# Kernel optimization log

Hardware: AMD Instinct MI355X
Metric: run time of the kernel (lower is better)

## Reference

```python
import jax, jax.numpy as jnp
import numpy as np

B = 8
A = 180      # num_angles
D = 512      # det_count
IMG = 512    # img_size


def _forward(x):
    # --- Ram-Lak filter in frequency domain ---
    freq = jnp.abs(jnp.fft.rfftfreq(D)).astype(jnp.float32)            # [D//2+1]
    filtered = jnp.fft.irfft(jnp.fft.rfft(x, axis=-1) * freq, n=D, axis=-1)  # [B,A,D]

    # --- precompute per-angle detector coordinates for every pixel ---
    lin = jnp.linspace(-1.0, 1.0, IMG, dtype=jnp.float32)
    yy, xx = jnp.meshgrid(lin, lin, indexing='ij')
    xxf = xx.reshape(-1)                                               # [HW]
    yyf = yy.reshape(-1)
    angles = jnp.linspace(0.0, np.pi - np.pi / A, A, dtype=jnp.float32)
    t = (xxf[None, :] * jnp.cos(angles)[:, None]
         + yyf[None, :] * jnp.sin(angles)[:, None]) / np.sqrt(2.0)     # [A,HW]
    u = jnp.clip((t + 1.0) * 0.5 * (D - 1.0), 0.0, D - 1.0)
    idx0 = jnp.floor(u).astype(jnp.int32)
    idx1 = jnp.minimum(idx0 + 1, D - 1)
    w = u - idx0.astype(jnp.float32)

    # --- backprojection sweep: scan over angles, accumulate in-register ---
    proj = jnp.transpose(filtered, (1, 0, 2))                          # [A,B,D]

    def step(acc, inputs):
        p, i0, i1, wa = inputs                                         # p:[B,D], i*/wa:[HW]
        s = jnp.take(p, i0, axis=1) * (1.0 - wa) + jnp.take(p, i1, axis=1) * wa
        return acc + s, None

    bn = x.shape[0]
    acc0 = jnp.zeros((bn, IMG * IMG), dtype=jnp.float32)
    acc, _ = jax.lax.scan(step, acc0, (proj, idx0, idx1, w))

    det_pixel_size = 2.0 / float(D)
    fbp = acc.reshape(bn, 1, IMG, IMG) * (det_pixel_size * np.pi / float(A))

    # --- 3x3 gaussian blur (sigma=0.5), depthwise on single channel ---
    coords = jnp.arange(-1, 2, dtype=jnp.float32)
    k1 = jnp.exp(-0.5 * (coords / 0.5) ** 2)
    k1 = k1 / k1.sum()
    k2 = jnp.outer(k1, k1)[None, None]                                 # [1,1,3,3] OIHW
    fbp = jax.lax.conv_general_dilated(fbp, k2, (1, 1), 'SAME')
    return jnp.clip(fbp, -1.0, 1.0)


def setup_inputs() -> dict:
    key = jax.random.key(0)
    x = jax.random.normal(key, (B, A, D), dtype=jnp.float32)
    return {"x": x, "input_is_sinogram": 1}


def reference(x, input_is_sinogram):
    # input_is_sinogram is a constant flag (True path): x is the sinogram [B,A,D].
    return _forward(x)
```

## Files before the change

### kernel.cpp

```cpp
#include <hip/hip_runtime.h>
#include <hip/hip_fp16.h>
#include <math.h>

#define NDET 512
#define NANG 180
#define NB   8
#define NIMG 512

#define WS_CASA 0
#define WS_CBT  360
#define WS_FGH  46464
#define WS_BP   (46464 + 368640)

typedef _Float16 h2_t __attribute__((ext_vector_type(2)));

__device__ __forceinline__ void gld_lds16(const void* g, void* l) {
    __builtin_amdgcn_global_load_lds((__attribute__((address_space(1))) void*)g,
                                     (__attribute__((address_space(3))) void*)l,
                                     16, 0, 0);
}

__device__ __forceinline__ int hswz(int s) {
    return (s & 0x78) | ((s ^ (s >> 3)) & 7);
}

__global__ __launch_bounds__(256) void k_filter(const float* __restrict__ x, float* ws) {
    __shared__ float xs[8 * 516];
    __shared__ float hrs[512];
    const int a     = blockIdx.x >> 1;
    const int half_ = blockIdx.x & 1;
    const int tid   = threadIdx.x;
    const int lane  = tid & 63;
    const int wv    = tid >> 6;

    #pragma unroll
    for (int p = 0; p < 2; ++p) {
        int n = tid + 256 * p;
        float h;
        if (n == 0) h = 0.25f;
        else if ((n & 1) == 0) h = 0.0f;
        else {
            double th = (double)n * (M_PI / 256.0);
            double s2 = sin(0.5 * th);
            double S  = (254.0 - 256.0 * cos(th)) / (4.0 * s2 * s2);
            h = (float)((2.0 * S - 256.0) / 262144.0);
        }
        hrs[hswz(n >> 2) * 4 + (n & 3)] = h;
    }
    {
        int b  = wv * 2 + (lane >> 5);
        int l5 = lane & 31;
        const float* xr = x + (b * NANG + a) * NDET;
        float* xd = xs + b * 516;
        #pragma unroll
        for (int p = 0; p < 4; ++p) {
            int idx = l5 * 4 + p * 128;
            *(float4*)(xd + idx) = *(const float4*)(xr + idx);
        }
    }
    if (half_ == 0) {
        double th = (double)a * (M_PI / 180.0);
        double sc = 255.5 / sqrt(2.0);
        const float ca = (float)(cos(th) * sc), sa = (float)(sin(th) * sc);
        if (tid == 0) {
            ws[WS_CASA + 2 * a]     = ca;
            ws[WS_CASA + 2 * a + 1] = sa;
        }
        const int bx = tid & 15, by = tid >> 4;
        const float x0 = -1.f + (float)(bx * 32)      * (2.f / 511.f);
        const float x1 = -1.f + (float)(bx * 32 + 31) * (2.f / 511.f);
        const float y0 = -1.f + (float)(by * 32)      * (2.f / 511.f);
        const float y1 = -1.f + (float)(by * 32 + 31) * (2.f / 511.f);
        float u00 = fmaf(x0, ca, fmaf(y0, sa, 255.5f));
        float u01 = fmaf(x1, ca, fmaf(y0, sa, 255.5f));
        float u10 = fmaf(x0, ca, fmaf(y1, sa, 255.5f));
        float u11 = fmaf(x1, ca, fmaf(y1, sa, 255.5f));
        float umin = fminf(fminf(u00, u01), fminf(u10, u11));
        int d0 = (int)floorf(umin) - 1;
        d0 = max(0, min(476, d0));
        ws[WS_CBT + tid * 180 + a] = 255.5f - (float)d0;
    }
    __syncthreads();

    const int b  = lane & 7;
    const int t  = lane >> 3;
    const int n0 = half_ * 256 + wv * 64 + t * 8;
    const int q  = n0 >> 2;
    const float* xrow = xs + b * 516;

    float acc[8] = {0, 0, 0, 0, 0, 0, 0, 0};
    float win[12];
    {
        int s2 = (-q - 2) & 127;
        int s1 = (-q - 1) & 127;
        float4 h2 = *(const float4*)(hrs + hswz(s2) * 4);
        float4 h1 = *(const float4*)(hrs + hswz(s1) * 4);
        win[0] = h2.x; win[1] = h2.y; win[2]  = h2.z; win[3]  = h2.w;
        win[4] = h1.x; win[5] = h1.y; win[6]  = h1.z; win[7]  = h1.w;
    }
    #pragma unroll 2
    for (int c = 0; c < 128; ++c) {
        int s = (c - q) & 127;
        float4 hc = *(const float4*)(hrs + hswz(s) * 4);
        win[8] = hc.x; win[9] = hc.y; win[10] = hc.z; win[11] = hc.w;
        float4 xv = *(const float4*)(xrow + c * 4);
        float xa[4] = {xv.x, xv.y, xv.z, xv.w};
        #pragma unroll
        for (int k = 0; k < 8; ++k)
            #pragma unroll
            for (int j = 0; j < 4; ++j)
                acc[k] = fmaf(xa[j], win[8 + j - k], acc[k]);
        #pragma unroll
        for (int i2 = 0; i2 < 8; ++i2) win[i2] = win[i2 + 4];
    }
    __half* fgh = (__half*)(ws + WS_FGH);
    #pragma unroll
    for (int k = 0; k < 8; ++k)
        fgh[(a * NDET + n0 + k) * NB + b] = __float2half(acc[k]);
}

#define WWIN 36
#define NCHK (NANG * WWIN)

__global__ __launch_bounds__(1024) void k_bp(float* ws) {
    __shared__ uint4 win4[NCHK];
    const int tid  = threadIdx.x;
    const int wv   = tid >> 6, lane = tid & 63;
    const int bid  = blockIdx.x;
    const int bx   = bid & 15, by = bid >> 4;
    const int iy   = by * 32 + (wv >> 2) * 8 + (lane >> 3);
    const int ix   = bx * 32 + (wv & 3) * 8 + (lane & 7);
    const float xf = -1.0f + (float)ix * (2.0f / 511.0f);
    const float yf = -1.0f + (float)iy * (2.0f / 511.0f);

    const __half* __restrict__ fgh  = (const __half*)(ws + WS_FGH);
    const float*  __restrict__ cbt  = ws + WS_CBT + bid * 180;
    const float*  __restrict__ casa = ws + WS_CASA;

    #pragma unroll
    for (int r = 0; r < 7; ++r) {
        int c = r * 1024 + tid;
        if (c < NCHK) {
            unsigned a = (unsigned)c / 36u;
            int o  = c - (int)a * 36;
            float cb = cbt[a];
            int d0 = (int)(255.5f - cb);
            gld_lds16(fgh + ((int)a * NDET + d0 + o) * NB, win4 + c);
        }
    }
    __syncthreads();

    float acc[8] = {0, 0, 0, 0, 0, 0, 0, 0};
    #pragma unroll 4
    for (int al = 0; al < NANG; ++al) {
        const float2 cs = *(const float2*)(casa + 2 * al);
        const float  cb = cbt[al];
        float v = fmaf(xf, cs.x, fmaf(yf, cs.y, cb));
        v = __builtin_amdgcn_fmed3f(v, 0.0f, 34.99996948f);
        float fj = floorf(v);
        float w  = v - fj;
        int  j0  = (int)fj;
        const char* pc = (const char*)win4 + al * (WWIN * 16) + (j0 << 4);
        uint4 da = *(const uint4*)pc;
        uint4 db = *(const uint4*)(pc + 16);
#if __has_builtin(__builtin_amdgcn_fdot2) && __has_builtin(__builtin_amdgcn_perm) && __has_builtin(__builtin_amdgcn_cvt_pkrtz)
        h2_t wp = __builtin_bit_cast(h2_t, __builtin_amdgcn_cvt_pkrtz(1.0f - w, w));
        unsigned pl0 = __builtin_amdgcn_perm(db.x, da.x, 0x05040100u);
        unsigned ph0 = __builtin_amdgcn_perm(db.x, da.x, 0x07060302u);
        unsigned pl1 = __builtin_amdgcn_perm(db.y, da.y, 0x05040100u);
        unsigned ph1 = __builtin_amdgcn_perm(db.y, da.y, 0x07060302u);
        unsigned pl2 = __builtin_amdgcn_perm(db.z, da.z, 0x05040100u);
        unsigned ph2 = __builtin_amdgcn_perm(db.z, da.z, 0x07060302u);
        unsigned pl3 = __builtin_amdgcn_perm(db.w, da.w, 0x05040100u);
        unsigned ph3 = __builtin_amdgcn_perm(db.w, da.w, 0x07060302u);
        acc[0] = __builtin_amdgcn_fdot2(__builtin_bit_cast(h2_t, pl0), wp, acc[0], false);
        acc[1] = __builtin_amdgcn_fdot2(__builtin_bit_cast(h2_t, ph0), wp, acc[1], false);
        acc[2] = __builtin_amdgcn_fdot2(__builtin_bit_cast(h2_t, pl1), wp, acc[2], false);
        acc[3] = __builtin_amdgcn_fdot2(__builtin_bit_cast(h2_t, ph1), wp, acc[3], false);
        acc[4] = __builtin_amdgcn_fdot2(__builtin_bit_cast(h2_t, pl2), wp, acc[4], false);
        acc[5] = __builtin_amdgcn_fdot2(__builtin_bit_cast(h2_t, ph2), wp, acc[5], false);
        acc[6] = __builtin_amdgcn_fdot2(__builtin_bit_cast(h2_t, pl3), wp, acc[6], false);
        acc[7] = __builtin_amdgcn_fdot2(__builtin_bit_cast(h2_t, ph3), wp, acc[7], false);
#else
        __half2 w2 = __float2half2_rn(w);
        __half2 a0 = __builtin_bit_cast(__half2, da.x), b0 = __builtin_bit_cast(__half2, db.x);
        __half2 a1 = __builtin_bit_cast(__half2, da.y), b1 = __builtin_bit_cast(__half2, db.y);
        __half2 a2 = __builtin_bit_cast(__half2, da.z), b2 = __builtin_bit_cast(__half2, db.z);
        __half2 a3 = __builtin_bit_cast(__half2, da.w), b3 = __builtin_bit_cast(__half2, db.w);
        float2 f0 = __half22float2(__hfma2(w2, __hsub2(b0, a0), a0));
        float2 f1 = __half22float2(__hfma2(w2, __hsub2(b1, a1), a1));
        float2 f2 = __half22float2(__hfma2(w2, __hsub2(b2, a2), a2));
        float2 f3 = __half22float2(__hfma2(w2, __hsub2(b3, a3), a3));
        acc[0] += f0.x; acc[1] += f0.y;
        acc[2] += f1.x; acc[3] += f1.y;
        acc[4] += f2.x; acc[5] += f2.y;
        acc[6] += f3.x; acc[7] += f3.y;
#endif
    }

    const float scale = (float)((2.0 / 512.0) * M_PI / 180.0);
    float* bp = ws + WS_BP;
    #pragma unroll
    for (int b = 0; b < 8; ++b)
        bp[b * (NIMG * NIMG) + iy * NIMG + ix] = acc[b] * scale;
}

__global__ __launch_bounds__(256) void k_blur(const float* __restrict__ ws, float* __restrict__ out) {
    const int gid = blockIdx.x * 256 + threadIdx.x;
    const int b  = gid >> 18;
    const int r  = (gid >> 9) & 511;
    const int cx = gid & 511;
    const float KA = 0.10650697891920077f;
    const float KB = 0.78698604216159850f;
    const float* img = ws + WS_BP + b * (NIMG * NIMG);
    const float* rp = img + r * 512 + cx;

    float rowm = 0.0f, row0, rowp = 0.0f;
    {
        float l  = (cx > 0)   ? rp[-1] : 0.0f;
        float rr = (cx < 511) ? rp[1]  : 0.0f;
        row0 = KA * (l + rr) + KB * rp[0];
    }
    if (r > 0) {
        const float* q = rp - 512;
        float l  = (cx > 0)   ? q[-1] : 0.0f;
        float rr = (cx < 511) ? q[1]  : 0.0f;
        rowm = KA * (l + rr) + KB * q[0];
    }
    if (r < 511) {
        const float* q = rp + 512;
        float l  = (cx > 0)   ? q[-1] : 0.0f;
        float rr = (cx < 511) ? q[1]  : 0.0f;
        rowp = KA * (l + rr) + KB * q[0];
    }
    float v = KA * (rowm + rowp) + KB * row0;
    v = fminf(fmaxf(v, -1.0f), 1.0f);
    out[gid] = v;
}

extern "C" void kernel_launch(void* const* d_in, const int* in_sizes, int n_in,
                              void* d_out, int out_size, void* d_ws, size_t ws_size,
                              hipStream_t stream) {
    const float* x = (const float*)d_in[0];
    float* out = (float*)d_out;
    float* ws  = (float*)d_ws;

    k_filter<<<NANG * 2, 256, 0, stream>>>(x, ws);
    k_bp<<<256, 1024, 0, stream>>>(ws);
    k_blur<<<(NB * NIMG * NIMG) / 256, 256, 0, stream>>>(ws, out);
}
```

Baseline: 77.90 us.

## Split backprojection angles across two blocks per tile with atomic accumulation

Each 32x32 pixel tile's angle loop is now split into two halves of 90 angles, which doubles the grid to 512 blocks. Each block stages half as much LDS window data, and its partial sums go into a zero-initialised buffer through atomicAdd. The detector window is also tightened from 36 to 34 entries by removing the -1 margin. The intent is better CU occupancy and smaller LDS footprint, at the cost of an extra memset, atomic traffic, and a tighter window that could clip edge samples.

```diff
diff --git a/kernel.cpp b/kernel.cpp
--- a/kernel.cpp
+++ b/kernel.cpp
@@ -76,8 +76,8 @@
         float u10 = fmaf(x0, ca, fmaf(y1, sa, 255.5f));
         float u11 = fmaf(x1, ca, fmaf(y1, sa, 255.5f));
         float umin = fminf(fminf(u00, u01), fminf(u10, u11));
-        int d0 = (int)floorf(umin) - 1;
-        d0 = max(0, min(476, d0));
+        int d0 = (int)floorf(umin);
+        d0 = max(0, min(NDET - 34, d0));
         ws[WS_CBT + tid * 180 + a] = 255.5f - (float)d0;
     }
     __syncthreads();
@@ -119,51 +119,54 @@
         fgh[(a * NDET + n0 + k) * NB + b] = __float2half(acc[k]);
 }
 
-#define WWIN 36
-#define NCHK (NANG * WWIN)
-
-__global__ __launch_bounds__(1024) void k_bp(float* ws) {
+#define WWIN 34
+#define CHANG 90
+#define NCHK (CHANG * WWIN)
+
+__global__ __launch_bounds__(1024, 8) void k_bp(float* ws) {
     __shared__ uint4 win4[NCHK];
     const int tid  = threadIdx.x;
     const int wv   = tid >> 6, lane = tid & 63;
-    const int bid  = blockIdx.x;
-    const int bx   = bid & 15, by = bid >> 4;
+    const int tile = blockIdx.x & 255;
+    const int ah   = (blockIdx.x >> 8) * CHANG;
+    const int bx   = tile & 15, by = tile >> 4;
     const int iy   = by * 32 + (wv >> 2) * 8 + (lane >> 3);
     const int ix   = bx * 32 + (wv & 3) * 8 + (lane & 7);
     const float xf = -1.0f + (float)ix * (2.0f / 511.0f);
     const float yf = -1.0f + (float)iy * (2.0f / 511.0f);
 
     const __half* __restrict__ fgh  = (const __half*)(ws + WS_FGH);
-    const float*  __restrict__ cbt  = ws + WS_CBT + bid * 180;
+    const float*  __restrict__ cbt  = ws + WS_CBT + tile * 180;
     const float*  __restrict__ casa = ws + WS_CASA;
 
     #pragma unroll
-    for (int r = 0; r < 7; ++r) {
+    for (int r = 0; r < 3; ++r) {
         int c = r * 1024 + tid;
         if (c < NCHK) {
-            unsigned a = (unsigned)c / 36u;
-            int o  = c - (int)a * 36;
-            float cb = cbt[a];
+            unsigned a = (unsigned)c / 34u;
+            int o  = c - (int)a * 34;
+            int ag = ah + (int)a;
+            float cb = cbt[ag];
             int d0 = (int)(255.5f - cb);
-            gld_lds16(fgh + ((int)a * NDET + d0 + o) * NB, win4 + c);
+            gld_lds16(fgh + (ag * NDET + d0 + o) * NB, win4 + c);
         }
     }
     __syncthreads();
 
     float acc[8] = {0, 0, 0, 0, 0, 0, 0, 0};
     #pragma unroll 4
-    for (int al = 0; al < NANG; ++al) {
-        const float2 cs = *(const float2*)(casa + 2 * al);
-        const float  cb = cbt[al];
+    for (int al = 0; al < CHANG; ++al) {
+        const int ag = ah + al;
+        const float2 cs = *(const float2*)(casa + 2 * ag);
+        const float  cb = cbt[ag];
         float v = fmaf(xf, cs.x, fmaf(yf, cs.y, cb));
-        v = __builtin_amdgcn_fmed3f(v, 0.0f, 34.99996948f);
+        v = __builtin_amdgcn_fmed3f(v, 0.0f, 32.99996948f);
         float fj = floorf(v);
         float w  = v - fj;
         int  j0  = (int)fj;
         const char* pc = (const char*)win4 + al * (WWIN * 16) + (j0 << 4);
         uint4 da = *(const uint4*)pc;
         uint4 db = *(const uint4*)(pc + 16);
-#if __has_builtin(__builtin_amdgcn_fdot2) && __has_builtin(__builtin_amdgcn_perm) && __has_builtin(__builtin_amdgcn_cvt_pkrtz)
         h2_t wp = __builtin_bit_cast(h2_t, __builtin_amdgcn_cvt_pkrtz(1.0f - w, w));
         unsigned pl0 = __builtin_amdgcn_perm(db.x, da.x, 0x05040100u);
         unsigned ph0 = __builtin_amdgcn_perm(db.x, da.x, 0x07060302u);
@@ -181,28 +184,13 @@
         acc[5] = __builtin_amdgcn_fdot2(__builtin_bit_cast(h2_t, ph2), wp, acc[5], false);
         acc[6] = __builtin_amdgcn_fdot2(__builtin_bit_cast(h2_t, pl3), wp, acc[6], false);
         acc[7] = __builtin_amdgcn_fdot2(__builtin_bit_cast(h2_t, ph3), wp, acc[7], false);
-#else
-        __half2 w2 = __float2half2_rn(w);
-        __half2 a0 = __builtin_bit_cast(__half2, da.x), b0 = __builtin_bit_cast(__half2, db.x);
-        __half2 a1 = __builtin_bit_cast(__half2, da.y), b1 = __builtin_bit_cast(__half2, db.y);
-        __half2 a2 = __builtin_bit_cast(__half2, da.z), b2 = __builtin_bit_cast(__half2, db.z);
-        __half2 a3 = __builtin_bit_cast(__half2, da.w), b3 = __builtin_bit_cast(__half2, db.w);
-        float2 f0 = __half22float2(__hfma2(w2, __hsub2(b0, a0), a0));
-        float2 f1 = __half22float2(__hfma2(w2, __hsub2(b1, a1), a1));
-        float2 f2 = __half22float2(__hfma2(w2, __hsub2(b2, a2), a2));
-        float2 f3 = __half22float2(__hfma2(w2, __hsub2(b3, a3), a3));
-        acc[0] += f0.x; acc[1] += f0.y;
-        acc[2] += f1.x; acc[3] += f1.y;
-        acc[4] += f2.x; acc[5] += f2.y;
-        acc[6] += f3.x; acc[7] += f3.y;
-#endif
     }
 
     const float scale = (float)((2.0 / 512.0) * M_PI / 180.0);
     float* bp = ws + WS_BP;
     #pragma unroll
     for (int b = 0; b < 8; ++b)
-        bp[b * (NIMG * NIMG) + iy * NIMG + ix] = acc[b] * scale;
+        atomicAdd(&bp[b * (NIMG * NIMG) + iy * NIMG + ix], acc[b] * scale);
 }
 
 __global__ __launch_bounds__(256) void k_blur(const float* __restrict__ ws, float* __restrict__ out) {
@@ -246,6 +234,7 @@
     float* ws  = (float*)d_ws;
 
     k_filter<<<NANG * 2, 256, 0, stream>>>(x, ws);
-    k_bp<<<256, 1024, 0, stream>>>(ws);
+    hipMemsetAsync(ws + WS_BP, 0, (size_t)NB * NIMG * NIMG * sizeof(float), stream);
+    k_bp<<<512, 1024, 0, stream>>>(ws);
     k_blur<<<(NB * NIMG * NIMG) / 256, 256, 0, stream>>>(ws, out);
 }
```

Result: slower. 90.32 us (+15.9%).
